# Optimization experiments

Hardware: AMD Instinct MI355X
Metric: run time of the kernel (lower is better)

The kernel has to match this reference:

```python
import jax, jax.numpy as jnp
import numpy as np
import jax.scipy.signal as jss

SX, SY, C, K = 256, 256, 3, 10
C0 = [0, 0, 0, 1, 1, 1, 2, 2, 2, 0]
C1 = [[0, 1, 2, 9], [3, 4, 5], [6, 7, 8]]
DD, DT, SIGMA = 5, 0.2, 0.65

_KX = jnp.array([[-1., 0., 1.], [-2., 0., 2.], [-1., 0., 1.]])
_KY = _KX.T


def _conv2(A, Kf):
    # zero-padded 'same' 2D true convolution, vmapped over channel axis
    return jax.vmap(lambda a: jss.convolve2d(a, Kf, mode='same'), in_axes=2, out_axes=2)(A)


def sobel(A):
    # (X, Y, c) -> (X, Y, 2, c): [sobel_y, sobel_x] stacked on axis 2 (FlowLenia convention)
    return jnp.concatenate([_conv2(A, _KY)[:, :, None, :], _conv2(A, _KX)[:, :, None, :]], axis=2)


def growth(U, m, s):
    # bell(U,m,s)*2 - 1
    return jnp.exp(-((U - m) / s) ** 2 / 2.) * 2. - 1.


def get_kernels_fft(R, r, a, w, b):
    # FlowLenia kernel construction: ring distance -> smooth cutoff * sum-of-bumps, normalized, fft2(fftshift)
    mid = SX // 2
    xs = jnp.arange(-mid, mid, dtype=jnp.float32)
    D = jnp.sqrt(xs[:, None] ** 2 + xs[None, :] ** 2)            # (X, Y)
    Dk = D[..., None] / ((R + 15.) * r)                          # (X, Y, k)
    ker = (b * jnp.exp(-(Dk[..., None] - a) ** 2 / w)).sum(-1)   # (X, Y, k)
    sig = 0.5 * (jnp.tanh(-(Dk - 1.) * 10. / 2.) + 1.)           # sigmoid(-(D-1)*10)
    Kk = sig * ker
    nK = Kk / Kk.sum(axis=(0, 1), keepdims=True)
    return jnp.fft.fft2(jnp.fft.fftshift(nK, axes=(0, 1)), axes=(0, 1))


def _rt_apply(A, F):
    # Reintegration tracking with 'wall' border: flow-driven mass redistribution over a (2dd+1)^2 neighborhood
    ii = jnp.arange(SX, dtype=jnp.float32)
    pos = jnp.stack(jnp.meshgrid(ii, ii, indexing='ij'), axis=-1) + 0.5   # (X, Y, 2) cell centers
    ma = DD - SIGMA                                   # max flow magnitude
    mu = pos[..., None] + jnp.clip(DT * F, -ma, ma)   # (X, Y, 2, C) target centers
    mu = jnp.clip(mu, SIGMA, SX - SIGMA)              # wall border
    offs = jnp.arange(-DD, DD + 1)
    gx, gy = jnp.meshgrid(offs, offs, indexing='ij')
    dxs, dys = gx.reshape(-1), gy.reshape(-1)
    clip_hi = min(1., 2. * SIGMA)

    def step(dx, dy):
        Ar = jnp.roll(A, (dx, dy), axis=(0, 1))
        mur = jnp.roll(mu, (dx, dy), axis=(0, 1))
        dpmu = jnp.abs(pos[..., None] - mur)                                  # (X, Y, 2, C)
        sz = 0.5 - dpmu + SIGMA
        area = jnp.prod(jnp.clip(sz, 0., clip_hi), axis=2) / (4. * SIGMA ** 2)  # (X, Y, C)
        return Ar * area

    return jax.vmap(step)(dxs, dys).sum(axis=0)


def setup_inputs() -> dict:
    key = jax.random.key(0)
    ks = jax.random.split(key, 9)
    A = jax.random.uniform(ks[0], (SX, SY, C), dtype=jnp.float32)
    R = jax.random.uniform(ks[1], (), minval=2.0, maxval=25.0)
    r = jax.random.uniform(ks[2], (K,), minval=0.2, maxval=1.0)
    m = jax.random.uniform(ks[3], (K,), minval=0.05, maxval=0.5)
    s = jax.random.uniform(ks[4], (K,), minval=0.001, maxval=0.18)
    h = jax.random.uniform(ks[5], (K,), minval=0.01, maxval=1.0)
    a = jax.random.uniform(ks[6], (K, 3), minval=0.0, maxval=1.0)
    b = jax.random.uniform(ks[7], (K, 3), minval=0.001, maxval=1.0)
    w = jax.random.uniform(ks[8], (K, 3), minval=0.01, maxval=0.5)
    return dict(A=A, R=R, r=r, m=m, s=s, h=h, a=a, b=b, w=w)


def reference(A, R, r, m, s, h, a, b, w):
    fK = get_kernels_fft(R, r, a, w, b)                       # (X, Y, k) complex
    fA = jnp.fft.fft2(A, axes=(0, 1))
    fAk = fA[:, :, jnp.array(C0)]                             # (X, Y, k)
    U = jnp.real(jnp.fft.ifft2(fK * fAk, axes=(0, 1)))        # (X, Y, k)
    U = growth(U, m, s) * h
    U = jnp.dstack([U[:, :, C1[c]].sum(axis=-1) for c in range(C)])  # (X, Y, C)
    nabla_U = sobel(U)                                        # (X, Y, 2, C)
    nabla_A = sobel(A.sum(axis=-1, keepdims=True))            # (X, Y, 2, 1)
    alpha = jnp.clip((A[:, :, None, :] / C) ** 2, 0., 1.)     # (X, Y, 1, C)
    F = nabla_U * (1. - alpha) - nabla_A * alpha              # (X, Y, 2, C)
    return _rt_apply(A, F)
```

## Files before the change

kernel.cpp:

```cpp
#include <hip/hip_runtime.h>

#define NPIX 65536

#define WS_APLANE 0
#define WS_ASUM   (3*NPIX)
#define WS_KOFF   (4*NPIX)
#define WS_UACC   (14*NPIX)
#define WS_ROWS   (24*NPIX)
#define WS_X1RE   (25*NPIX)
#define WS_X1IM   (38*NPIX)
#define WS_YRE    (51*NPIX)
#define WS_YIM    (64*NPIX)
#define WS_END    (77*NPIX)


__device__ __forceinline__ void fft256_core(float* __restrict__ re, float* __restrict__ im,
                                            const float* __restrict__ twr,
                                            const float* __restrict__ twi, int lane) {
    #pragma unroll
    for (int s = 1; s <= 8; ++s) {
        int h = 1 << (s - 1);
        #pragma unroll
        for (int b = 0; b < 2; ++b) {
            int idx = b*64 + lane;
            int pos = idx & (h - 1);
            int g   = idx >> (s - 1);
            int i0 = (g << s) + pos;
            int i1 = i0 + h;
            int tj = pos << (8 - s);
            float wr = twr[tj], wi = twi[tj];
            float xr = re[i1], xi = im[i1];
            float br = fmaf(xr, wr, -xi*wi);
            float bi = fmaf(xr, wi,  xi*wr);
            float ar = re[i0], ai = im[i0];
            re[i0] = ar + br; im[i0] = ai + bi;
            re[i1] = ar - br; im[i1] = ai - bi;
        }
    }
}

__device__ inline void sobel_at(const float* __restrict__ p, int x, int y,
                                float& gy, float& gx) {
    float v[3][3];
    #pragma unroll
    for (int ii = -1; ii <= 1; ++ii)
        #pragma unroll
        for (int jj = -1; jj <= 1; ++jj) {
            int xx = x + ii, yy = y + jj;
            v[ii+1][jj+1] = (xx < 0 || xx > 255 || yy < 0 || yy > 255)
                            ? 0.0f : p[xx*256 + yy];
        }
    gy = (v[0][0] + 2.0f*v[0][1] + v[0][2]) - (v[2][0] + 2.0f*v[2][1] + v[2][2]);
    gx = (v[0][0] + 2.0f*v[1][0] + v[2][0]) - (v[0][2] + 2.0f*v[1][2] + v[2][2]);
}

__global__ void k_prep(const float* __restrict__ A, const float* __restrict__ R_,
                       const float* __restrict__ r_, const float* __restrict__ a_,
                       const float* __restrict__ b_, const float* __restrict__ w_,
                       float* __restrict__ ws) {
    __shared__ float red[4];
    int u = blockIdx.x;
    int t = threadIdx.x, wid = t >> 6, lane = t & 63;
    if (u < 256) {
        int idx = u*256 + t;
        float a0 = A[idx*3+0], a1 = A[idx*3+1], a2 = A[idx*3+2];
        ws[WS_APLANE + idx]          = a0;
        ws[WS_APLANE + NPIX + idx]   = a1;
        ws[WS_APLANE + 2*NPIX + idx] = a2;
        ws[WS_ASUM + idx] = a0 + a1 + a2;
        return;
    }
    int bk = u - 256;
    int k = bk >> 8, i = bk & 255;
    float R = R_[0];
    float denom = (R + 15.0f) * r_[k];
    int di = i - 128, dj = t - 128;
    float D  = sqrtf((float)(di*di + dj*dj));
    float Dk = D / denom;
    float v = 0.0f;
    if (Dk <= 3.0f) {
        float ker = 0.0f;
        #pragma unroll
        for (int tt = 0; tt < 3; ++tt) {
            float d = Dk - a_[k*3+tt];
            ker += b_[k*3+tt] * expf(-((d*d) / w_[k*3+tt]));
        }
        float sig = 1.0f / (1.0f + expf(10.0f * (Dk - 1.0f)));
        v = sig * ker;
    }
    int iw = (i + 128) & 255, jw = (t + 128) & 255;
    ws[WS_KOFF + k*NPIX + iw*256 + jw] = v;
    float ssum = v;
    #pragma unroll
    for (int off = 32; off; off >>= 1) ssum += __shfl_xor(ssum, off);
    __syncthreads();
    if (lane == 0) red[wid] = ssum;
    __syncthreads();
    if (t == 0) ws[WS_ROWS + k*256 + i] = red[0]+red[1]+red[2]+red[3];
}

__global__ __launch_bounds__(256) void k_fft1(float* __restrict__ ws) {
    __shared__ float buf[2048];
    __shared__ float twr[128], twi[128];
    int t = threadIdx.x, wid = t >> 6, lane = t & 63;
    if (t < 128) { float ang = (float)t * 0.0245436930f; twr[t] = cosf(ang); twi[t] = -sinf(ang); }
    __syncthreads();
    int p = blockIdx.x >> 6, lb = (blockIdx.x & 63) * 4;
    int f = 2*p, g = 2*p + 1;
    const float* frow = ws + ((f < 3) ? (WS_APLANE + f*NPIX) : (WS_KOFF + (f-3)*NPIX))
                      + (lb + wid)*256;
    const float* grow_ = (g < 13)
        ? ws + ((g < 3) ? (WS_APLANE + g*NPIX) : (WS_KOFF + (g-3)*NPIX)) + (lb + wid)*256
        : nullptr;
    float* re = buf + wid*512;
    float* im = re + 256;
    #pragma unroll
    for (int e = 0; e < 4; ++e) {
        int idx = e*64 + lane;
        int dst = __brev(idx) >> 24;
        re[dst] = frow[idx];
        im[dst] = grow_ ? grow_[idx] : 0.0f;
    }
    fft256_core(re, im, twr, twi, lane);
    __syncthreads();
    int u2 = (256 - t) & 255;
    float4 Fre, Fim, Gre, Gim;
    float* pF[4] = {&Fre.x, &Fim.x, &Gre.x, &Gim.x};
    #pragma unroll
    for (int l = 0; l < 4; ++l) {
        float zr1 = buf[l*512 + t],  zi1 = buf[l*512 + 256 + t];
        float zr2 = buf[l*512 + u2], zi2 = buf[l*512 + 256 + u2];
        pF[0][l] = 0.5f*(zr1 + zr2);
        pF[1][l] = 0.5f*(zi1 - zi2);
        pF[2][l] = 0.5f*(zi1 + zi2);
        pF[3][l] = 0.5f*(zr2 - zr1);
    }
    *(float4*)&ws[WS_X1RE + f*NPIX + t*256 + lb] = Fre;
    *(float4*)&ws[WS_X1IM + f*NPIX + t*256 + lb] = Fim;
    if (g < 13) {
        *(float4*)&ws[WS_X1RE + g*NPIX + t*256 + lb] = Gre;
        *(float4*)&ws[WS_X1IM + g*NPIX + t*256 + lb] = Gim;
    }
}

__global__ __launch_bounds__(512) void k_colfft_mul(float* __restrict__ ws) {
    __shared__ float hat[13*512];
    __shared__ float pk[5*512];
    __shared__ float twc[128], twsF[128], twsI[128];
    int ky = blockIdx.x;
    int t = threadIdx.x, wave = t >> 6, lane = t & 63;
    if (t < 128) {
        float ang = (float)t * 0.0245436930f;
        twc[t] = cosf(ang);
        float sv = sinf(ang);
        twsF[t] = -sv; twsI[t] = sv;
    }
    __syncthreads();
    const int rowbase = ky * 256;
    #pragma unroll
    for (int rep = 0; rep < 2; ++rep) {
        int p = (rep == 0) ? wave : (wave >= 3 ? wave + 5 : 13);
        if (p < 13) {
            float* re = &hat[p*512];
            float* im = re + 256;
            const float* rr = ws + WS_X1RE + p*NPIX + rowbase;
            const float* ri = ws + WS_X1IM + p*NPIX + rowbase;
            #pragma unroll
            for (int e = 0; e < 4; ++e) {
                int idx = e*64 + lane;
                int dst = __brev(idx) >> 24;
                re[dst] = rr[idx];
                im[dst] = ri[idx];
            }
            fft256_core(re, im, twc, twsF, lane);
        }
    }
    __syncthreads();
    if (wave < 5) {
        int j = wave;
        int ka = 2*j, kb = 2*j + 1;
        int ca = (ka < 9) ? ka/3 : 0;
        int cb = (kb < 9) ? kb/3 : 0;
        const float* Ar = &hat[ca*512];      const float* Ai = Ar + 256;
        const float* Kr = &hat[(3+ka)*512];  const float* Ki = Kr + 256;
        const float* Br = &hat[cb*512];      const float* Bi = Br + 256;
        const float* Lr = &hat[(3+kb)*512];  const float* Li = Lr + 256;
        float* re = &pk[j*512];
        float* im = re + 256;
        #pragma unroll
        for (int e = 0; e < 4; ++e) {
            int idx = e*64 + lane;
            int dst = __brev(idx) >> 24;
            float ar = Ar[idx], ai = Ai[idx];
            float kr = Kr[idx], ki = Ki[idx];
            float uar = ar*kr - ai*ki;
            float uai = ar*ki + ai*kr;
            float br = Br[idx], bi = Bi[idx];
            float lr = Lr[idx], li = Li[idx];
            float ubr = br*lr - bi*li;
            float ubi = br*li + bi*lr;
            re[dst] = uar - ubi;
            im[dst] = uai + ubr;
        }
        fft256_core(re, im, twc, twsI, lane);
        float* Yre = ws + WS_YRE + j*NPIX + ky;
        float* Yim = ws + WS_YIM + j*NPIX + ky;
        #pragma unroll
        for (int e = 0; e < 4; ++e) {
            int x = e*64 + lane;
            Yre[x*256] = re[x];
            Yim[x*256] = im[x];
        }
    }
}

__global__ __launch_bounds__(256) void k_ifft_y(float* __restrict__ ws) {
    __shared__ float buf[4*512];
    __shared__ float twc[128], twsI[128];
    int t = threadIdx.x, wid = t >> 6, lane = t & 63;
    if (t < 128) { float ang = (float)t * 0.0245436930f; twc[t] = cosf(ang); twsI[t] = sinf(ang); }
    __syncthreads();
    int j  = blockIdx.x >> 6;
    int lb = (blockIdx.x & 63) * 4;
    int x = lb + wid;
    float* re = &buf[wid*512];
    float* im = re + 256;
    const float* Yre = ws + WS_YRE + j*NPIX + x*256;
    const float* Yim = ws + WS_YIM + j*NPIX + x*256;
    #pragma unroll
    for (int e = 0; e < 4; ++e) {
        int ky = e*64 + lane;
        int dst = __brev(ky) >> 24;
        re[dst] = Yre[ky];
        im[dst] = Yim[ky];
    }
    fft256_core(re, im, twc, twsI, lane);
    const float sc = 1.0f / 65536.0f;
    float* Ua = ws + WS_UACC + (2*j)*NPIX   + x*256;
    float* Ub = ws + WS_UACC + (2*j+1)*NPIX + x*256;
    #pragma unroll
    for (int e = 0; e < 4; ++e) {
        int y = e*64 + lane;
        Ua[y] = re[y] * sc;
        Ub[y] = im[y] * sc;
    }
}

__global__ __launch_bounds__(256) void k_post(float* __restrict__ ws,
                                              const float* __restrict__ m_,
                                              const float* __restrict__ s_,
                                              const float* __restrict__ h_,
                                              float* __restrict__ out) {
    __shared__ float sU[13*256];
    __shared__ float sX[11*256], sY[11*256], sA[11*256];
    __shared__ float kinv[4];
    int b = blockIdx.x;
    int c = b >> 8, x = b & 255;
    int t = threadIdx.x, wid = t >> 6, lane = t & 63;
    int nk = (c == 0) ? 4 : 3;
    if (wid < nk) {
        int k = (wid == 3) ? 9 : c*3 + wid;
        const float* rw = ws + WS_ROWS + k*256;
        float v = rw[lane] + rw[64+lane] + rw[128+lane] + rw[192+lane];
        #pragma unroll
        for (int off = 32; off; off >>= 1) v += __shfl_xor(v, off);
        if (lane == 0) kinv[wid] = 1.0f / v;
    }
    __syncthreads();
    const float* uacc = ws + WS_UACC;
    for (int rr = 0; rr < 13; ++rr) {
        int ar = (x - 6 + rr) & 255;
        int idx = ar*256 + t;
        float outv = 0.0f;
        for (int kk = 0; kk < nk; ++kk) {
            int k = (kk == 3) ? 9 : c*3 + kk;
            float U = uacc[k*NPIX + idx] * kinv[kk];
            float z = (U - m_[k]) / s_[k];
            outv += h_[k] * (expf(-0.5f*z*z)*2.0f - 1.0f);
        }
        sU[rr*256 + t] = outv;
    }
    __syncthreads();
    int y = t;
    for (int i = 0; i < 11; ++i) {
        int w = (x - 5 + i) & 255;
        float gyA, gxA;
        sobel_at(ws + WS_ASUM, w, y, gyA, gxA);
        float v[3][3];
        #pragma unroll
        for (int ii = 0; ii < 3; ++ii) {
            bool zr = (ii == 0 && w == 0) || (ii == 2 && w == 255);
            #pragma unroll
            for (int jj = -1; jj <= 1; ++jj) {
                int yy = y + jj;
                v[ii][jj+1] = (zr || yy < 0 || yy > 255) ? 0.0f : sU[(i+ii)*256 + yy];
            }
        }
        float gy = (v[0][0] + 2.0f*v[0][1] + v[0][2]) - (v[2][0] + 2.0f*v[2][1] + v[2][2]);
        float gx = (v[0][0] + 2.0f*v[1][0] + v[2][0]) - (v[0][2] + 2.0f*v[1][2] + v[2][2]);
        float a = ws[WS_APLANE + c*NPIX + w*256 + y];
        float al = (a / 3.0f); al = al * al;
        al = fminf(fmaxf(al, 0.0f), 1.0f);
        float F0 = gy * (1.0f - al) - gyA * al;
        float F1 = gx * (1.0f - al) - gxA * al;
        float d0 = fminf(fmaxf(0.2f * F0, -4.35f), 4.35f);
        float d1 = fminf(fmaxf(0.2f * F1, -4.35f), 4.35f);
        sX[i*256 + y] = fminf(fmaxf((float)w + 0.5f + d0, 0.65f), 255.35f);
        sY[i*256 + y] = fminf(fmaxf((float)y + 0.5f + d1, 0.65f), 255.35f);
        sA[i*256 + y] = a;
    }
    __syncthreads();
    float px = (float)x + 0.5f, py = (float)y + 0.5f;
    float acc = 0.0f;
    #pragma unroll
    for (int dx = -5; dx <= 5; ++dx) {
        int rb = (5 - dx) * 256;
        for (int dy = -5; dy <= 5; ++dy) {
            int sy = (y - dy) & 255;
            float a  = sA[rb + sy];
            float ax = 1.15f - fabsf(px - sX[rb + sy]);
            float ay = 1.15f - fabsf(py - sY[rb + sy]);
            ax = fminf(fmaxf(ax, 0.0f), 1.0f);
            ay = fminf(fmaxf(ay, 0.0f), 1.0f);
            acc = fmaf(a, ax * ay, acc);
        }
    }
    out[(x*256 + y)*3 + c] = acc * (1.0f / (4.0f * 0.65f * 0.65f));
}

extern "C" void kernel_launch(void* const* d_in, const int* in_sizes, int n_in,
                              void* d_out, int out_size, void* d_ws, size_t ws_size,
                              hipStream_t stream) {
    const float* A = (const float*)d_in[0];
    const float* R = (const float*)d_in[1];
    const float* r = (const float*)d_in[2];
    const float* m = (const float*)d_in[3];
    const float* s = (const float*)d_in[4];
    const float* h = (const float*)d_in[5];
    const float* a = (const float*)d_in[6];
    const float* b = (const float*)d_in[7];
    const float* w = (const float*)d_in[8];
    float* ws  = (float*)d_ws;
    float* out = (float*)d_out;

    k_prep<<<2816, 256, 0, stream>>>(A, R, r, a, b, w, ws);
    k_fft1<<<448, 256, 0, stream>>>(ws);
    k_colfft_mul<<<256, 512, 0, stream>>>(ws);
    k_ifft_y<<<320, 256, 0, stream>>>(ws);
    k_post<<<768, 256, 0, stream>>>(ws, m, s, h, out);
}
```

Measured before the change: 134.0 us.

## Fuse kernel construction and A deinterleave into first row FFT kernel

Removes the separate prep kernel and computes the ring kernels and A-plane loads directly inside the first row-FFT kernel, writing per-row kernel sums there too. The A channel-sum plane is no longer stored globally; the post kernel builds it in shared memory from the three A planes over a 13-row halo. This cuts one launch and the global write/read of the 10 spatial kernel planes and the sum plane. In exchange, kernel evaluation (exp-heavy) now sits on the FFT blocks' critical path, and the post kernel uses more shared memory, which may lower occupancy.

```diff
diff --git a/kernel.cpp b/kernel.cpp
--- a/kernel.cpp
+++ b/kernel.cpp
@@ -3,8 +3,6 @@
 #define NPIX 65536
 
 #define WS_APLANE 0
-#define WS_ASUM   (3*NPIX)
-#define WS_KOFF   (4*NPIX)
 #define WS_UACC   (14*NPIX)
 #define WS_ROWS   (24*NPIX)
 #define WS_X1RE   (25*NPIX)
@@ -39,42 +37,12 @@
     }
 }
 
-__device__ inline void sobel_at(const float* __restrict__ p, int x, int y,
-                                float& gy, float& gx) {
-    float v[3][3];
-    #pragma unroll
-    for (int ii = -1; ii <= 1; ++ii)
-        #pragma unroll
-        for (int jj = -1; jj <= 1; ++jj) {
-            int xx = x + ii, yy = y + jj;
-            v[ii+1][jj+1] = (xx < 0 || xx > 255 || yy < 0 || yy > 255)
-                            ? 0.0f : p[xx*256 + yy];
-        }
-    gy = (v[0][0] + 2.0f*v[0][1] + v[0][2]) - (v[2][0] + 2.0f*v[2][1] + v[2][2]);
-    gx = (v[0][0] + 2.0f*v[1][0] + v[2][0]) - (v[0][2] + 2.0f*v[1][2] + v[2][2]);
-}
-
-__global__ void k_prep(const float* __restrict__ A, const float* __restrict__ R_,
-                       const float* __restrict__ r_, const float* __restrict__ a_,
-                       const float* __restrict__ b_, const float* __restrict__ w_,
-                       float* __restrict__ ws) {
-    __shared__ float red[4];
-    int u = blockIdx.x;
-    int t = threadIdx.x, wid = t >> 6, lane = t & 63;
-    if (u < 256) {
-        int idx = u*256 + t;
-        float a0 = A[idx*3+0], a1 = A[idx*3+1], a2 = A[idx*3+2];
-        ws[WS_APLANE + idx]          = a0;
-        ws[WS_APLANE + NPIX + idx]   = a1;
-        ws[WS_APLANE + 2*NPIX + idx] = a2;
-        ws[WS_ASUM + idx] = a0 + a1 + a2;
-        return;
-    }
-    int bk = u - 256;
-    int k = bk >> 8, i = bk & 255;
-    float R = R_[0];
+__device__ __forceinline__ float kval(int k, int di, int dj, float R,
+                                      const float* __restrict__ r_,
+                                      const float* __restrict__ a_,
+                                      const float* __restrict__ b_,
+                                      const float* __restrict__ w_) {
     float denom = (R + 15.0f) * r_[k];
-    int di = i - 128, dj = t - 128;
     float D  = sqrtf((float)(di*di + dj*dj));
     float Dk = D / denom;
     float v = 0.0f;
@@ -88,39 +56,66 @@
         float sig = 1.0f / (1.0f + expf(10.0f * (Dk - 1.0f)));
         v = sig * ker;
     }
-    int iw = (i + 128) & 255, jw = (t + 128) & 255;
-    ws[WS_KOFF + k*NPIX + iw*256 + jw] = v;
-    float ssum = v;
-    #pragma unroll
-    for (int off = 32; off; off >>= 1) ssum += __shfl_xor(ssum, off);
-    __syncthreads();
-    if (lane == 0) red[wid] = ssum;
-    __syncthreads();
-    if (t == 0) ws[WS_ROWS + k*256 + i] = red[0]+red[1]+red[2]+red[3];
-}
-
-__global__ __launch_bounds__(256) void k_fft1(float* __restrict__ ws) {
+    return v;
+}
+
+__global__ __launch_bounds__(256) void k_fft1x(const float* __restrict__ A,
+                                               const float* __restrict__ R_,
+                                               const float* __restrict__ r_,
+                                               const float* __restrict__ a_,
+                                               const float* __restrict__ b_,
+                                               const float* __restrict__ w_,
+                                               float* __restrict__ ws) {
     __shared__ float buf[2048];
     __shared__ float twr[128], twi[128];
     int t = threadIdx.x, wid = t >> 6, lane = t & 63;
     if (t < 128) { float ang = (float)t * 0.0245436930f; twr[t] = cosf(ang); twi[t] = -sinf(ang); }
-    __syncthreads();
     int p = blockIdx.x >> 6, lb = (blockIdx.x & 63) * 4;
     int f = 2*p, g = 2*p + 1;
-    const float* frow = ws + ((f < 3) ? (WS_APLANE + f*NPIX) : (WS_KOFF + (f-3)*NPIX))
-                      + (lb + wid)*256;
-    const float* grow_ = (g < 13)
-        ? ws + ((g < 3) ? (WS_APLANE + g*NPIX) : (WS_KOFF + (g-3)*NPIX)) + (lb + wid)*256
-        : nullptr;
+    int row = lb + wid;
+    float R = R_[0];
     float* re = buf + wid*512;
     float* im = re + 256;
+    int di = (row < 128) ? row : row - 256;
+    float sumf = 0.0f, sumg = 0.0f;
     #pragma unroll
     for (int e = 0; e < 4; ++e) {
         int idx = e*64 + lane;
         int dst = __brev(idx) >> 24;
-        re[dst] = frow[idx];
-        im[dst] = grow_ ? grow_[idx] : 0.0f;
-    }
+        int dj = (idx < 128) ? idx : idx - 256;
+        float vf, vg;
+        if (f < 3) {
+            vf = A[(row*256 + idx)*3 + f];
+            ws[WS_APLANE + f*NPIX + row*256 + idx] = vf;
+        } else {
+            vf = kval(f - 3, di, dj, R, r_, a_, b_, w_);
+            sumf += vf;
+        }
+        if (g < 13) {
+            if (g < 3) {
+                vg = A[(row*256 + idx)*3 + g];
+                ws[WS_APLANE + g*NPIX + row*256 + idx] = vg;
+            } else {
+                vg = kval(g - 3, di, dj, R, r_, a_, b_, w_);
+                sumg += vg;
+            }
+        } else vg = 0.0f;
+        re[dst] = vf;
+        im[dst] = vg;
+    }
+    if (f >= 3) {
+        float s = sumf;
+        #pragma unroll
+        for (int off = 32; off; off >>= 1) s += __shfl_xor(s, off);
+        if (lane == 0) ws[WS_ROWS + (f-3)*256 + row] = s;
+    }
+    if (g >= 3 && g < 13) {
+        float s = sumg;
+        #pragma unroll
+        for (int off = 32; off; off >>= 1) s += __shfl_xor(s, off);
+        if (lane == 0) ws[WS_ROWS + (g-3)*256 + row] = s;
+    }
+    __syncthreads();
     fft256_core(re, im, twr, twi, lane);
     __syncthreads();
     int u2 = (256 - t) & 255;
@@ -252,6 +247,7 @@
                                               const float* __restrict__ h_,
                                               float* __restrict__ out) {
     __shared__ float sU[13*256];
+    __shared__ float sAS[13*256];
     __shared__ float sX[11*256], sY[11*256], sA[11*256];
     __shared__ float kinv[4];
     int b = blockIdx.x;
@@ -266,6 +262,12 @@
         for (int off = 32; off; off >>= 1) v += __shfl_xor(v, off);
         if (lane == 0) kinv[wid] = 1.0f / v;
     }
+    const float* ap0 = ws + WS_APLANE;
+    for (int rr = 0; rr < 13; ++rr) {
+        int ar = (x - 6 + rr) & 255;
+        int idx = ar*256 + t;
+        sAS[rr*256 + t] = ap0[idx] + ap0[NPIX + idx] + ap0[2*NPIX + idx];
+    }
     __syncthreads();
     const float* uacc = ws + WS_UACC;
     for (int rr = 0; rr < 13; ++rr) {
@@ -284,20 +286,22 @@
     int y = t;
     for (int i = 0; i < 11; ++i) {
         int w = (x - 5 + i) & 255;
-        float gyA, gxA;
-        sobel_at(ws + WS_ASUM, w, y, gyA, gxA);
-        float v[3][3];
+        float vv[3][3], vA[3][3];
         #pragma unroll
         for (int ii = 0; ii < 3; ++ii) {
             bool zr = (ii == 0 && w == 0) || (ii == 2 && w == 255);
             #pragma unroll
             for (int jj = -1; jj <= 1; ++jj) {
                 int yy = y + jj;
-                v[ii][jj+1] = (zr || yy < 0 || yy > 255) ? 0.0f : sU[(i+ii)*256 + yy];
+                bool zz = zr || yy < 0 || yy > 255;
+                vv[ii][jj+1] = zz ? 0.0f : sU[(i+ii)*256 + yy];
+                vA[ii][jj+1] = zz ? 0.0f : sAS[(i+ii)*256 + yy];
             }
         }
-        float gy = (v[0][0] + 2.0f*v[0][1] + v[0][2]) - (v[2][0] + 2.0f*v[2][1] + v[2][2]);
-        float gx = (v[0][0] + 2.0f*v[1][0] + v[2][0]) - (v[0][2] + 2.0f*v[1][2] + v[2][2]);
+        float gy  = (vv[0][0] + 2.0f*vv[0][1] + vv[0][2]) - (vv[2][0] + 2.0f*vv[2][1] + vv[2][2]);
+        float gx  = (vv[0][0] + 2.0f*vv[1][0] + vv[2][0]) - (vv[0][2] + 2.0f*vv[1][2] + vv[2][2]);
+        float gyA = (vA[0][0] + 2.0f*vA[0][1] + vA[0][2]) - (vA[2][0] + 2.0f*vA[2][1] + vA[2][2]);
+        float gxA = (vA[0][0] + 2.0f*vA[1][0] + vA[2][0]) - (vA[0][2] + 2.0f*vA[1][2] + vA[2][2]);
         float a = ws[WS_APLANE + c*NPIX + w*256 + y];
         float al = (a / 3.0f); al = al * al;
         al = fminf(fmaxf(al, 0.0f), 1.0f);
@@ -343,8 +347,7 @@
     float* ws  = (float*)d_ws;
     float* out = (float*)d_out;
 
-    k_prep<<<2816, 256, 0, stream>>>(A, R, r, a, b, w, ws);
-    k_fft1<<<448, 256, 0, stream>>>(ws);
+    k_fft1x<<<448, 256, 0, stream>>>(A, R, r, a, b, w, ws);
     k_colfft_mul<<<256, 512, 0, stream>>>(ws);
     k_ifft_y<<<320, 256, 0, stream>>>(ws);
     k_post<<<768, 256, 0, stream>>>(ws, m, s, h, out);
```

Measured after the change: 137.9 us. 2.9% more time.
